# Optimization experiments

Hardware: AMD Instinct MI355X
Metric: run time of the kernel (lower is better)

## Reference

```python
import jax, jax.numpy as jnp
import numpy as np

D = 256

def setup_inputs() -> dict:
    key = jax.random.key(0)
    ks = iter(jax.random.split(key, 40))
    def nrm(shape, s=0.05):
        return (jax.random.normal(next(ks), shape, dtype=jnp.float32) * s)
    inp = {}
    inp['prot_data'] = jax.random.normal(next(ks), (8, 1000, 768), dtype=jnp.float32)
    inp['drug_data_ver'] = jax.random.normal(next(ks), (8, 56, 43), dtype=jnp.float32)
    inp['drug_data_adj'] = jax.random.uniform(next(ks), (8, 56, 56), dtype=jnp.float32)
    inp['prot_contacts'] = jax.random.uniform(next(ks), (8, 1000, 1000), dtype=jnp.float32)
    inp['prot_inter'] = jax.random.uniform(next(ks), (8, 1000, 56), dtype=jnp.float32)
    inp['prot_inter_exist'] = jax.random.uniform(next(ks), (8,), dtype=jnp.float32)
    inp['label'] = jax.random.normal(next(ks), (8, 1), dtype=jnp.float32)
    inp['fused_matrix'] = jax.random.normal(next(ks), (999, 1000), dtype=jnp.float32)
    # params
    inp['W_prot'] = nrm((768, D)); inp['b_prot'] = jnp.zeros((D,), jnp.float32)
    inp['gcn_W0'] = nrm((43, D));  inp['gcn_b0'] = jnp.zeros((D,), jnp.float32)
    inp['gcn_W1'] = nrm((D, D));   inp['gcn_b1'] = jnp.zeros((D,), jnp.float32)
    inp['gcn_W2'] = nrm((D, D));   inp['gcn_b2'] = jnp.zeros((D,), jnp.float32)
    inp['gcn_Wf'] = nrm((D, D));   inp['gcn_bf'] = jnp.zeros((D,), jnp.float32)
    inp['Wjp'] = nrm((D, D)); inp['bjp'] = jnp.zeros((D,), jnp.float32)
    inp['Wjc'] = nrm((D, D)); inp['bjc'] = jnp.zeros((D,), jnp.float32)
    inp['conv_w'] = nrm((64, 1, 4)); inp['conv_b'] = jnp.zeros((64,), jnp.float32)
    inp['W_r1'] = nrm((64 * 32, 600)); inp['b_r1'] = jnp.zeros((600,), jnp.float32)
    inp['W_r2'] = nrm((600, 300));     inp['b_r2'] = jnp.zeros((300,), jnp.float32)
    inp['W_r3'] = nrm((300, 1));       inp['b_r3'] = jnp.zeros((1,), jnp.float32)
    return inp

LAM_L1 = 1.0; LAM_FUSED = 1.0; LAM_GROUP = 1.0; LAM_BIND = 1.0

def reference(prot_data, drug_data_ver, drug_data_adj, prot_contacts, prot_inter,
              prot_inter_exist, label, fused_matrix,
              W_prot, b_prot, gcn_W0, gcn_b0, gcn_W1, gcn_b1, gcn_W2, gcn_b2,
              gcn_Wf, gcn_bf, Wjp, bjp, Wjc, bjc, conv_w, conv_b,
              W_r1, b_r1, W_r2, b_r2, W_r3, b_r3):
    # protein embedding (active path: single linear)
    prot = prot_data @ W_prot + b_prot                      # (b, 1000, 256)
    # compound GCN
    x = drug_data_ver
    for W, b in ((gcn_W0, gcn_b0), (gcn_W1, gcn_b1), (gcn_W2, gcn_b2)):
        x = jax.nn.relu(jnp.einsum('bij,bjd->bid', drug_data_adj, x @ W + b))
    comp = x @ gcn_Wf + gcn_bf                              # (b, 56, 256)
    # joint attention over prot x comp
    qp = jax.nn.relu(prot) @ Wjp + bjp
    qc = jax.nn.relu(comp) @ Wjc + bjc
    inter = jax.nn.sigmoid(jnp.einsum('bid,bkd->bik', qp, qc))  # (b, 1000, 56)
    inter = inter / jnp.sum(inter, axis=(1, 2), keepdims=True)
    # outer-product bilinear attention + weighted reduction (the 4D intermediate)
    cp4 = jnp.tanh(prot[:, :, None, :] * comp[:, None, :, :])   # (b, 1000, 56, 256)
    cp = jnp.einsum('bikd,bik->bd', cp4, inter)                 # (b, 256)
    h = cp[:, None, :]                                          # (b, 1, 256) NCH
    h = jax.lax.conv_general_dilated(h, conv_w, (2,), [(1, 1)],
                                     dimension_numbers=('NCH', 'OIH', 'NCH'))
    h = h + conv_b[None, :, None]                               # (b, 64, 128)
    h = jax.nn.leaky_relu(h, 0.1)
    h = jax.lax.reduce_window(h, -jnp.inf, jax.lax.max,
                              (1, 1, 4), (1, 1, 4), 'VALID')    # (b, 64, 32)
    h = h.reshape(h.shape[0], 64 * 32)
    h = jax.nn.leaky_relu(h @ W_r1 + b_r1, 0.1)
    h = jax.nn.leaky_relu(h @ W_r2 + b_r2, 0.1)
    affn = h @ W_r3 + b_r3                                      # (b, 1)
    # losses
    reg_l1 = jnp.mean(jnp.sum(jnp.abs(inter), axis=(1, 2)))
    reg_fused = jnp.mean(jnp.sum(jnp.abs(jnp.einsum('bij,ti->bjt', inter, fused_matrix)), axis=(1, 2)))
    group = jnp.sum(jnp.einsum('bij,bki->bjk', inter ** 2, prot_contacts), axis=1)  # (b, 1000)
    group = jnp.where(group == 0, group + 1e10, group)
    reg_group = jnp.mean(jnp.sum(jnp.sqrt(group) * jnp.sqrt(jnp.sum(prot_contacts, axis=2)), axis=1))
    loss0 = LAM_L1 * reg_l1 + LAM_FUSED * reg_fused + LAM_GROUP * reg_group
    lab_inter = prot_inter_exist[:, None, None] * prot_inter
    loss1 = jnp.mean(jnp.sqrt(jnp.sum((inter - lab_inter) ** 2, axis=(1, 2)))) * LAM_BIND
    loss2 = jnp.mean((affn - label) ** 2)
    return loss0 + loss1 + loss2
```

## Files before the change

### kernel.cpp

```cpp
#include <hip/hip_runtime.h>
#include <hip/hip_bf16.h>
#include <math.h>

#define B 8
#define NP 1000
#define NK 56
#define DP 768
#define DV 43
#define DD 256
#define NT 999

typedef __attribute__((ext_vector_type(8))) short bf16x8;
typedef __attribute__((ext_vector_type(4))) float f32x4;

__device__ inline short f2bf(float x) {
    __hip_bfloat16 h = __float2bfloat16(x);
    return __builtin_bit_cast(short, h);
}


template<bool RELU_IN>
__device__ __forceinline__ void gemm_body(
    const float* __restrict__ A, const short* __restrict__ Wb,
    const float* __restrict__ bias, float* __restrict__ C,
    int N, int K, int bm, int bn, int tid) {
    int lane = tid & 63, w = tid >> 6;
    int m0 = bm * 32 + (w >> 1) * 16;
    int n0 = bn * 128 + (w & 1) * 64;
    int lrow = lane & 15, lk = lane >> 4;
    f32x4 acc[4] = {{0.f,0.f,0.f,0.f},{0.f,0.f,0.f,0.f},
                    {0.f,0.f,0.f,0.f},{0.f,0.f,0.f,0.f}};
    const float* arow = A + (size_t)(m0 + lrow) * K + lk * 8;
    for (int k0 = 0; k0 < K; k0 += 32) {
        f32x4 a0 = *reinterpret_cast<const f32x4*>(arow + k0);
        f32x4 a1 = *reinterpret_cast<const f32x4*>(arow + k0 + 4);
        bf16x8 af;
        #pragma unroll
        for (int e = 0; e < 4; ++e) {
            float v0 = a0[e], v1 = a1[e];
            if (RELU_IN) { v0 = fmaxf(v0, 0.f); v1 = fmaxf(v1, 0.f); }
            af[e] = f2bf(v0); af[4 + e] = f2bf(v1);
        }
        const short* bbase = Wb + ((size_t)((k0 >> 3) + lk) * N + n0 + lrow) * 8;
        #pragma unroll
        for (int nt = 0; nt < 4; ++nt) {
            bf16x8 bf = *reinterpret_cast<const bf16x8*>(bbase + nt * 128);
            acc[nt] = __builtin_amdgcn_mfma_f32_16x16x32_bf16(af, bf, acc[nt], 0, 0, 0);
        }
    }
    #pragma unroll
    for (int nt = 0; nt < 4; ++nt) {
        int col = n0 + nt * 16 + lrow;
        float bv = bias[col];
        #pragma unroll
        for (int r = 0; r < 4; ++r) {
            int row = m0 + lk * 4 + r;
            C[(size_t)row * N + col] = acc[nt][r] + bv;
        }
    }
}

__device__ __forceinline__ void gcn_layer_body(
    const float* __restrict__ x, const float* __restrict__ adj,
    const float* __restrict__ W, const float* __restrict__ bias,
    float* __restrict__ y, int KIN, int bi, int tid,
    float* arow, float* u) {
    int b = bi / NK, i = bi % NK;
    if (tid < NK) arow[tid] = adj[((size_t)b * NK + i) * NK + tid];
    __syncthreads();
    if (tid < KIN) {
        float a0 = 0.f, a1 = 0.f;
        for (int j = 0; j < NK; j += 2) {
            a0 = fmaf(arow[j],     x[((size_t)b * NK + j)     * KIN + tid], a0);
            a1 = fmaf(arow[j + 1], x[((size_t)b * NK + j + 1) * KIN + tid], a1);
        }
        u[tid] = a0 + a1;
    }
    float rs = 0.f;
    for (int j = 0; j < NK; ++j) rs += arow[j];
    __syncthreads();
    float a0 = 0.f, a1 = 0.f, a2 = 0.f, a3 = 0.f;
    int kk = 0;
    for (; kk + 4 <= KIN; kk += 4) {
        a0 = fmaf(u[kk],     W[(size_t)kk * DD + tid],       a0);
        a1 = fmaf(u[kk + 1], W[(size_t)(kk + 1) * DD + tid], a1);
        a2 = fmaf(u[kk + 2], W[(size_t)(kk + 2) * DD + tid], a2);
        a3 = fmaf(u[kk + 3], W[(size_t)(kk + 3) * DD + tid], a3);
    }
    for (; kk < KIN; ++kk) a0 = fmaf(u[kk], W[(size_t)kk * DD + tid], a0);
    float v = a0 + a1 + a2 + a3 + rs * bias[tid];
    y[((size_t)b * NK + i) * DD + tid] = fmaxf(v, 0.f);
}

__device__ __forceinline__ void gcn_tail_body(
    const float* __restrict__ y1, const float* __restrict__ adj,
    const float* __restrict__ W2, const float* __restrict__ b2,
    const float* __restrict__ Wf, const float* __restrict__ bf,
    const float* __restrict__ Wjc, const float* __restrict__ bjc,
    float* __restrict__ comp, float* __restrict__ qcout,
    int bi, int tid, float* arow, float* u) {
    int b = bi / NK, i = bi % NK;
    if (tid < NK) arow[tid] = adj[((size_t)b * NK + i) * NK + tid];
    __syncthreads();
    {
        float a0 = 0.f, a1 = 0.f;
        for (int j = 0; j < NK; j += 2) {
            a0 = fmaf(arow[j],     y1[((size_t)b * NK + j)     * DD + tid], a0);
            a1 = fmaf(arow[j + 1], y1[((size_t)b * NK + j + 1) * DD + tid], a1);
        }
        u[tid] = a0 + a1;
    }
    float rs = 0.f;
    for (int j = 0; j < NK; ++j) rs += arow[j];
    __syncthreads();
    float a0 = 0.f, a1 = 0.f, a2 = 0.f, a3 = 0.f;
    #pragma unroll 4
    for (int kk = 0; kk < DD; kk += 4) {
        a0 = fmaf(u[kk],     W2[(size_t)kk * DD + tid],       a0);
        a1 = fmaf(u[kk + 1], W2[(size_t)(kk + 1) * DD + tid], a1);
        a2 = fmaf(u[kk + 2], W2[(size_t)(kk + 2) * DD + tid], a2);
        a3 = fmaf(u[kk + 3], W2[(size_t)(kk + 3) * DD + tid], a3);
    }
    float y2 = fmaxf(a0 + a1 + a2 + a3 + rs * b2[tid], 0.f);
    __syncthreads();
    u[tid] = y2;
    __syncthreads();
    a0 = a1 = a2 = a3 = 0.f;
    #pragma unroll 4
    for (int kk = 0; kk < DD; kk += 4) {
        a0 = fmaf(u[kk],     Wf[(size_t)kk * DD + tid],       a0);
        a1 = fmaf(u[kk + 1], Wf[(size_t)(kk + 1) * DD + tid], a1);
        a2 = fmaf(u[kk + 2], Wf[(size_t)(kk + 2) * DD + tid], a2);
        a3 = fmaf(u[kk + 3], Wf[(size_t)(kk + 3) * DD + tid], a3);
    }
    float cv = a0 + a1 + a2 + a3 + bf[tid];
    comp[((size_t)b * NK + i) * DD + tid] = cv;
    __syncthreads();
    u[tid] = fmaxf(cv, 0.f);
    __syncthreads();
    a0 = a1 = a2 = a3 = 0.f;
    #pragma unroll 4
    for (int kk = 0; kk < DD; kk += 4) {
        a0 = fmaf(u[kk],     Wjc[(size_t)kk * DD + tid],       a0);
        a1 = fmaf(u[kk + 1], Wjc[(size_t)(kk + 1) * DD + tid], a1);
        a2 = fmaf(u[kk + 2], Wjc[(size_t)(kk + 2) * DD + tid], a2);
        a3 = fmaf(u[kk + 3], Wjc[(size_t)(kk + 3) * DD + tid], a3);
    }
    qcout[((size_t)b * NK + i) * DD + tid] = a0 + a1 + a2 + a3 + bjc[tid];
}

__global__ __launch_bounds__(256) void k1_kernel(
    const float* __restrict__ W_prot, short* __restrict__ Wb1,
    const float* __restrict__ Wjp, short* __restrict__ Wb2,
    const float* __restrict__ fusedM, short* __restrict__ fMb,
    float* __restrict__ zero_region,
    const float* __restrict__ drug_ver, const float* __restrict__ adj,
    const float* __restrict__ W0, const float* __restrict__ b0,
    float* __restrict__ y0) {
    __shared__ float smem[2112];
    int blk = blockIdx.x, tid = threadIdx.x;
    if (blk < 96) {
        int idx = blk * 256 + tid;
        int koct = idx / DD, n = idx % DD;
        bf16x8 v;
        #pragma unroll
        for (int e = 0; e < 8; ++e)
            v[e] = f2bf(W_prot[(size_t)(koct * 8 + e) * DD + n]);
        *reinterpret_cast<bf16x8*>(Wb1 + (size_t)idx * 8) = v;
    } else if (blk < 128) {
        int idx = (blk - 96) * 256 + tid;
        int koct = idx / DD, n = idx % DD;
        bf16x8 v;
        #pragma unroll
        for (int e = 0; e < 8; ++e)
            v[e] = f2bf(Wjp[(size_t)(koct * 8 + e) * DD + n]);
        *reinterpret_cast<bf16x8*>(Wb2 + (size_t)idx * 8) = v;
    } else if (blk < 640) {
        int blk2 = blk - 128;
        int t0 = (blk2 >> 3) * 16;
        int i0 = (blk2 & 7) * 128;
        for (int l = tid; l < 16 * 128; l += 256) {
            int tt = l >> 7, ii = l & 127;
            int t = t0 + tt, i = i0 + ii;
            smem[tt * 132 + ii] = (t < NT && i < NP) ? fusedM[(size_t)t * NP + i] : 0.f;
        }
        __syncthreads();
        int octl = tid >> 4, tl = tid & 15;
        bf16x8 v;
        #pragma unroll
        for (int e = 0; e < 8; ++e)
            v[e] = f2bf(smem[tl * 132 + octl * 8 + e]);
        size_t oct = i0 / 8 + octl;
        *reinterpret_cast<bf16x8*>(fMb + (oct * 1024 + t0 + tl) * 8) = v;
    } else if (blk < 677) {
        int idx = (blk - 640) * 256 + tid;
        if (idx < 48 + B * 600 + B * 300 + B * DD) zero_region[idx] = 0.f;
    } else {
        gcn_layer_body(drug_ver, adj, W0, b0, y0, DV, blk - 677, tid,
                       smem, smem + 64);
    }
}

__global__ __launch_bounds__(256) void k2_kernel(
    const float* __restrict__ prot_data, const short* __restrict__ Wb1,
    const float* __restrict__ b_prot, float* __restrict__ prot,
    const float* __restrict__ y0, const float* __restrict__ adj,
    const float* __restrict__ W1, const float* __restrict__ b1,
    float* __restrict__ y1) {
    __shared__ float smem[320];
    int blk = blockIdx.x, tid = threadIdx.x;
    if (blk < 500)
        gemm_body<false>(prot_data, Wb1, b_prot, prot, DD, DP, blk >> 1, blk & 1, tid);
    else
        gcn_layer_body(y0, adj, W1, b1, y1, DD, blk - 500, tid, smem, smem + 64);
}

__global__ __launch_bounds__(256) void k3_kernel(
    const float* __restrict__ prot, const short* __restrict__ Wb2,
    const float* __restrict__ bjp, float* __restrict__ qp,
    const float* __restrict__ y1, const float* __restrict__ adj,
    const float* __restrict__ W2, const float* __restrict__ b2,
    const float* __restrict__ Wf, const float* __restrict__ bf,
    const float* __restrict__ Wjc, const float* __restrict__ bjc,
    float* __restrict__ comp, float* __restrict__ qc) {
    __shared__ float smem[320];
    int blk = blockIdx.x, tid = threadIdx.x;
    if (blk < 500)
        gemm_body<true>(prot, Wb2, bjp, qp, DD, DD, blk >> 1, blk & 1, tid);
    else
        gcn_tail_body(y1, adj, W2, b2, Wf, bf, Wjc, bjc, comp, qc,
                      blk - 500, tid, smem, smem + 64);
}

__global__ __launch_bounds__(256) void inter_all_kernel(
    const float* __restrict__ qp, const float* __restrict__ qc,
    const float* __restrict__ prot_inter, const float* __restrict__ exist,
    float* __restrict__ inter, float* __restrict__ s_bi,
    short* __restrict__ iTb, float* __restrict__ accums) {
    int b = blockIdx.x / 125, chunk = blockIdx.x % 125;
    __shared__ float qcT[DD * 57];
    __shared__ float qpS[8][DD];
    __shared__ float vS[8][57];
    __shared__ float wred[4][4];
    int tid = threadIdx.x;
    for (int l = tid; l < NK * DD; l += 256) {
        int k = l / DD, d = l % DD;
        qcT[d * 57 + k] = qc[((size_t)b * NK + k) * DD + d];
    }
    for (int l = tid; l < 8 * DD; l += 256) {
        int r = l >> 8, d = l & 255;
        qpS[r][d] = qp[((size_t)b * NP + chunk * 8 + r) * DD + d];
    }
    __syncthreads();
    int w = tid >> 6, lane = tid & 63;
    float ex = exist[b];
    int r0 = w * 2, r1 = w * 2 + 1;
    float acc0 = 0.f, acc1 = 0.f;
    if (lane < NK) {
        #pragma unroll 8
        for (int d = 0; d < DD; ++d) {
            float c = qcT[d * 57 + lane];
            acc0 = fmaf(qpS[r0][d], c, acc0);
            acc1 = fmaf(qpS[r1][d], c, acc1);
        }
    }
    float aV = 0.f, aA = 0.f, aC = 0.f, aD = 0.f;
    #pragma unroll
    for (int ii = 0; ii < 2; ++ii) {
        int i = chunk * 8 + w * 2 + ii;
        float v = 0.f, lab = 0.f;
        if (lane < NK) {
            float acc = (ii == 0) ? acc0 : acc1;
            v = 1.f / (1.f + __expf(-acc));
            lab = ex * prot_inter[((size_t)b * NP + i) * NK + lane];
            inter[((size_t)b * NP + i) * NK + lane] = v;
            vS[w * 2 + ii][lane] = v;
        }
        float v2 = v * v;
        float r = v2;
        #pragma unroll
        for (int off = 32; off; off >>= 1) r += __shfl_down(r, off);
        if (lane == 0) s_bi[(size_t)b * NP + i] = r;
        aV += v; aA += v2; aC += v * lab; aD += lab * lab;
    }
    #pragma unroll
    for (int off = 32; off; off >>= 1) {
        aV += __shfl_down(aV, off);
        aA += __shfl_down(aA, off);
        aC += __shfl_down(aC, off);
        aD += __shfl_down(aD, off);
    }
    if (lane == 0) {
        wred[w][0] = aV; wred[w][1] = aA; wred[w][2] = aC; wred[w][3] = aD;
    }
    __syncthreads();
    if (tid < 4) {
        float s = wred[0][tid] + wred[1][tid] + wred[2][tid] + wred[3][tid];
        atomicAdd(&accums[tid * 8 + b], s);
    }
    if (tid < NK) {
        bf16x8 pk;
        #pragma unroll
        for (int e = 0; e < 8; ++e) pk[e] = f2bf(vS[e][tid]);
        *reinterpret_cast<bf16x8*>(iTb + ((size_t)chunk * 448 + b * NK + tid) * 8) = pk;
        if (chunk == 124) {
            bf16x8 z = {0,0,0,0,0,0,0,0};
            #pragma unroll
            for (int oct = 125; oct < 128; ++oct)
                *reinterpret_cast<bf16x8*>(iTb + ((size_t)oct * 448 + b * NK + tid) * 8) = z;
        }
    }
}

__global__ __launch_bounds__(256) void k5_kernel(
    const float* __restrict__ prot, const float* __restrict__ comp,
    const float* __restrict__ inter, float* __restrict__ cp,
    const short* __restrict__ iTb, const short* __restrict__ fMb,
    float* __restrict__ fusedAbs,
    const float* __restrict__ contacts, const float* __restrict__ s_bi,
    const float* __restrict__ accums, float* __restrict__ groupv) {
    __shared__ float irow[8][NK];
    __shared__ float sb[8];
    int blk = blockIdx.x, tid = threadIdx.x;
    if (blk < 1000) {
        int b = blk / 125, chunk = blk % 125;
        int d = tid;
        float creg[NK];
        #pragma unroll
        for (int k = 0; k < NK; ++k)
            creg[k] = comp[((size_t)b * NK + k) * DD + d];
        for (int l = tid; l < 8 * NK; l += 256) {
            int ii = l / NK, k = l % NK;
            irow[ii][k] = inter[((size_t)b * NP + chunk * 8 + ii) * NK + k];
        }
        const float C2LOG2E = 2.8853900817779268f;
        float p2l[8];
        #pragma unroll
        for (int ii = 0; ii < 8; ++ii)
            p2l[ii] = C2LOG2E * prot[((size_t)b * NP + chunk * 8 + ii) * DD + d];
        __syncthreads();
        float acc0 = 0.f, acc1 = 0.f;
        #pragma unroll 1
        for (int ii = 0; ii < 8; ++ii) {
            float p = p2l[ii];
            #pragma unroll
            for (int k = 0; k < NK; k += 2) {
                float e0 = __builtin_amdgcn_exp2f(p * creg[k]);
                float e1 = __builtin_amdgcn_exp2f(p * creg[k + 1]);
                float r0 = __builtin_amdgcn_rcpf(e0 + 1.f);
                float r1 = __builtin_amdgcn_rcpf(e1 + 1.f);
                acc0 = fmaf(fmaf(-2.f, r0, 1.f), irow[ii][k],     acc0);
                acc1 = fmaf(fmaf(-2.f, r1, 1.f), irow[ii][k + 1], acc1);
            }
        }
        atomicAdd(&cp[(size_t)b * DD + d], acc0 + acc1);
    } else if (blk < 1112) {
        int fblk = blk - 1000;
        int mb = fblk % 14, nb = fblk / 14;
        int lane = tid & 63, w = tid >> 6;
        if (tid < 8) sb[tid] = 0.f;
        __syncthreads();
        int m0 = mb * 32 + (w >> 1) * 16;
        int n0 = nb * 128 + (w & 1) * 64;
        int lrow = lane & 15, lk = lane >> 4;
        f32x4 acc[4] = {{0.f,0.f,0.f,0.f},{0.f,0.f,0.f,0.f},
                        {0.f,0.f,0.f,0.f},{0.f,0.f,0.f,0.f}};
        for (int koct0 = 0; koct0 < 128; koct0 += 4) {
            int koct = koct0 + lk;
            bf16x8 af = *reinterpret_cast<const bf16x8*>(
                iTb + ((size_t)koct * 448 + m0 + lrow) * 8);
            const short* bb = fMb + ((size_t)koct * 1024 + n0 + lrow) * 8;
            #pragma unroll
            for (int nt = 0; nt < 4; ++nt) {
                bf16x8 bf = *reinterpret_cast<const bf16x8*>(bb + nt * 128);
                acc[nt] = __builtin_amdgcn_mfma_f32_16x16x32_bf16(af, bf, acc[nt], 0, 0, 0);
            }
        }
        #pragma unroll
        for (int r = 0; r < 4; ++r) {
            float part = fabsf(acc[0][r]) + fabsf(acc[1][r]) +
                         fabsf(acc[2][r]) + fabsf(acc[3][r]);
            #pragma unroll
            for (int off = 1; off < 16; off <<= 1)
                part += __shfl_xor(part, off);
            if (lrow == 0) {
                int row = m0 + lk * 4 + r;
                atomicAdd(&sb[row / NK], part);
            }
        }
        __syncthreads();
        if (tid < 8 && sb[tid] != 0.f) atomicAdd(&fusedAbs[tid], sb[tid]);
    } else {
        int w = tid >> 6, lane = tid & 63;
        int gk = (blk - 1112) * 4 + w;
        int b = gk / NP;
        const f32x4* row4 = reinterpret_cast<const f32x4*>(
            contacts + (size_t)gk * NP);
        const f32x4* sv4 = reinterpret_cast<const f32x4*>(s_bi + (size_t)b * NP);
        f32x4 z = {0.f, 0.f, 0.f, 0.f};
        f32x4 c0 = row4[lane];
        f32x4 c1 = row4[lane + 64];
        f32x4 c2 = row4[lane + 128];
        f32x4 c3 = z, s3 = z;
        f32x4 s0 = sv4[lane];
        f32x4 s1 = sv4[lane + 64];
        f32x4 s2 = sv4[lane + 128];
        if (lane + 192 < 250) { c3 = row4[lane + 192]; s3 = sv4[lane + 192]; }
        float g0 = 0.f, g1 = 0.f, g2 = 0.f, g3 = 0.f;
        #pragma unroll
        for (int e = 0; e < 4; ++e) {
            g0 = fmaf(c0[e], s0[e], g0);
            g1 = fmaf(c1[e], s1[e], g1);
            g2 = fmaf(c2[e], s2[e], g2);
            g3 = fmaf(c3[e], s3[e], g3);
        }
        float r0 = (c0[0] + c0[1]) + (c0[2] + c0[3]);
        float r1 = (c1[0] + c1[1]) + (c1[2] + c1[3]);
        float r2 = (c2[0] + c2[1]) + (c2[2] + c2[3]);
        float r3 = (c3[0] + c3[1]) + (c3[2] + c3[3]);
        float g = (g0 + g1) + (g2 + g3);
        float rs = (r0 + r1) + (r2 + r3);
        #pragma unroll
        for (int off = 32; off; off >>= 1) {
            g += __shfl_down(g, off);
            rs += __shfl_down(rs, off);
        }
        if (lane == 0) {
            float val;
            if (g == 0.f) val = sqrtf(1e10f) * sqrtf(rs);
            else          val = sqrtf(g) / accums[b] * sqrtf(rs);
            groupv[gk] = val;
        }
    }
}

__global__ __launch_bounds__(256) void convpool_kernel(
    const float* __restrict__ cp, const float* __restrict__ accums,
    const float* __restrict__ conv_w, const float* __restrict__ conv_b,
    float* __restrict__ pooled) {
    int b = blockIdx.x, t = threadIdx.x;
    __shared__ float xS[258];
    __shared__ float convo[8192];
    float invS = 1.f / accums[b];
    xS[t + 1] = cp[(size_t)b * DD + t] * invS;
    if (t == 0) { xS[0] = 0.f; xS[257] = 0.f; }
    __syncthreads();
    for (int l = t; l < 8192; l += 256) {
        int o = l >> 7, pos = l & 127;
        float acc = conv_b[o];
        int base = pos * 2;
        #pragma unroll
        for (int h = 0; h < 4; ++h)
            acc = fmaf(xS[base + h], conv_w[o * 4 + h], acc);
        convo[l] = (acc > 0.f) ? acc : 0.1f * acc;
    }
    __syncthreads();
    for (int l = t; l < 2048; l += 256) {
        int o = l >> 5, p = l & 31;
        float m = convo[o * 128 + p * 4];
        m = fmaxf(m, convo[o * 128 + p * 4 + 1]);
        m = fmaxf(m, convo[o * 128 + p * 4 + 2]);
        m = fmaxf(m, convo[o * 128 + p * 4 + 3]);
        pooled[b * 2048 + l] = m;
    }
}

template<bool FIN>
__global__ __launch_bounds__(256) void fc_partial_kernel(
    const float* __restrict__ in, const float* __restrict__ bias_in,
    const float* __restrict__ W, float* __restrict__ raw,
    int K, int N, int kchunk) {
    int t = threadIdx.x;
    int ol = t & 63;
    int o = blockIdx.x * 64 + ol;
    int w = t >> 6;
    int kbeg = blockIdx.y * kchunk;
    int kend = kbeg + kchunk; if (kend > K) kend = K;
    int len = kend - kbeg;
    __shared__ float sin_[B][128];
    for (int l = t; l < B * len; l += 256) {
        int b = l / len, k = l % len;
        float v = in[(size_t)b * K + kbeg + k];
        if (FIN) {
            v += bias_in[kbeg + k];
            v = (v > 0.f) ? v : 0.1f * v;
        }
        sin_[b][k] = v;
    }
    __syncthreads();
    float acc[B];
    #pragma unroll
    for (int b = 0; b < B; ++b) acc[b] = 0.f;
    if (o < N) {
        for (int k = kbeg + w; k < kend; k += 4) {
            float wv = W[(size_t)k * N + o];
            int kl = k - kbeg;
            #pragma unroll
            for (int b = 0; b < B; ++b)
                acc[b] = fmaf(sin_[b][kl], wv, acc[b]);
        }
    }
    __shared__ float red[4][64][B];
    #pragma unroll
    for (int b = 0; b < B; ++b) red[w][ol][b] = acc[b];
    __syncthreads();
    for (int p = t; p < 64 * B; p += 256) {
        int oo = p / B, b = p % B;
        int o2 = blockIdx.x * 64 + oo;
        if (o2 < N) {
            float s = red[0][oo][b] + red[1][oo][b] + red[2][oo][b] + red[3][oo][b];
            atomicAdd(&raw[(size_t)b * N + o2], s);
        }
    }
}

__global__ __launch_bounds__(256) void final_kernel(
    const float* __restrict__ accums, const float* __restrict__ groupv,
    const float* __restrict__ raw2, const float* __restrict__ b_r2,
    const float* __restrict__ W3, const float* __restrict__ b3,
    const float* __restrict__ label, float* __restrict__ out) {
    int tid = threadIdx.x;
    __shared__ float affnS[8];
    {
        int b = tid >> 5, k0 = tid & 31;
        float acc = 0.f;
        for (int k = k0; k < 300; k += 32) {
            float v = raw2[(size_t)b * 300 + k] + b_r2[k];
            v = (v > 0.f) ? v : 0.1f * v;
            acc = fmaf(v, W3[k], acc);
        }
        #pragma unroll
        for (int off = 16; off; off >>= 1) acc += __shfl_down(acc, off);
        if (k0 == 0) affnS[b] = acc + b3[0];
    }
    float s = 0.f;
    for (int l = tid; l < B * NP; l += 256) s += groupv[l];
    __shared__ float r[256];
    r[tid] = s;
    __syncthreads();
    for (int st = 128; st; st >>= 1) {
        if (tid < st) r[tid] += r[tid + st];
        __syncthreads();
    }
    if (tid == 0) {
        float gtot = r[0];
        float l0 = 0.f, l1 = 0.f, l2 = 0.f;
        for (int b = 0; b < B; ++b) {
            float S = accums[b];
            float A = accums[8 + b], C = accums[16 + b], D = accums[24 + b];
            float fA = accums[32 + b];
            l0 += 1.f + fA / S;
            float bind = A / (S * S) - 2.f * C / S + D;
            l1 += sqrtf(fmaxf(bind, 0.f));
            float dd = affnS[b] - label[b];
            l2 += dd * dd;
        }
        out[0] = (l0 + gtot + l1 + l2) * 0.125f;
    }
}

extern "C" void kernel_launch(void* const* d_in, const int* in_sizes, int n_in,
                              void* d_out, int out_size, void* d_ws, size_t ws_size,
                              hipStream_t stream) {
    const float* prot_data   = (const float*)d_in[0];
    const float* drug_ver    = (const float*)d_in[1];
    const float* drug_adj    = (const float*)d_in[2];
    const float* contacts    = (const float*)d_in[3];
    const float* prot_inter  = (const float*)d_in[4];
    const float* exist       = (const float*)d_in[5];
    const float* label       = (const float*)d_in[6];
    const float* fused       = (const float*)d_in[7];
    const float* W_prot      = (const float*)d_in[8];
    const float* b_prot      = (const float*)d_in[9];
    const float* gcn_W0      = (const float*)d_in[10];
    const float* gcn_b0      = (const float*)d_in[11];
    const float* gcn_W1      = (const float*)d_in[12];
    const float* gcn_b1      = (const float*)d_in[13];
    const float* gcn_W2      = (const float*)d_in[14];
    const float* gcn_b2      = (const float*)d_in[15];
    const float* gcn_Wf      = (const float*)d_in[16];
    const float* gcn_bf      = (const float*)d_in[17];
    const float* Wjp         = (const float*)d_in[18];
    const float* bjp         = (const float*)d_in[19];
    const float* Wjc         = (const float*)d_in[20];
    const float* bjc         = (const float*)d_in[21];
    const float* conv_w      = (const float*)d_in[22];
    const float* conv_b      = (const float*)d_in[23];
    const float* W_r1        = (const float*)d_in[24];
    const float* b_r1        = (const float*)d_in[25];
    const float* W_r2        = (const float*)d_in[26];
    const float* b_r2        = (const float*)d_in[27];
    const float* W_r3        = (const float*)d_in[28];
    const float* b_r3        = (const float*)d_in[29];

    float* ws = (float*)d_ws;
    size_t off = 0;
    auto alloc = [&](size_t n) { float* p = ws + off; off += n; return p; };
    float* prot     = alloc((size_t)B * NP * DD);
    float* qp       = alloc((size_t)B * NP * DD);
    float* tbuf     = alloc((size_t)B * NK * DD);
    float* ybuf     = alloc((size_t)B * NK * DD);
    float* comp     = alloc((size_t)B * NK * DD);
    float* qc       = alloc((size_t)B * NK * DD);
    float* inter    = alloc((size_t)B * NP * NK);
    float* s_bi     = alloc((size_t)B * NP);
    float* pooled   = alloc((size_t)B * 2048);
    float* groupv   = alloc((size_t)B * NP);
    short* Wb1      = (short*)alloc((DP / 8) * DD * 8 / 2);
    short* Wb2      = (short*)alloc((DD / 8) * DD * 8 / 2);
    short* fMb      = (short*)alloc((size_t)128 * 1024 * 8 / 2);
    float* accums   = alloc(48);
    float* raw1     = alloc((size_t)B * 600);
    float* raw2     = alloc((size_t)B * 300);
    float* cp       = alloc((size_t)B * DD);

    short* iTb = (short*)tbuf;
    (void)ybuf;

    k1_kernel<<<1125, 256, 0, stream>>>(W_prot, Wb1, Wjp, Wb2, fused, fMb,
                                        accums, drug_ver, drug_adj,
                                        gcn_W0, gcn_b0, tbuf);

    k2_kernel<<<948, 256, 0, stream>>>(prot_data, Wb1, b_prot, prot,
                                       tbuf, drug_adj, gcn_W1, gcn_b1, ybuf);

    k3_kernel<<<948, 256, 0, stream>>>(prot, Wb2, bjp, qp,
                                       ybuf, drug_adj, gcn_W2, gcn_b2,
                                       gcn_Wf, gcn_bf, Wjc, bjc, comp, qc);

    inter_all_kernel<<<B * 125, 256, 0, stream>>>(
        qp, qc, prot_inter, exist, inter, s_bi, iTb, accums);

    k5_kernel<<<3112, 256, 0, stream>>>(prot, comp, inter, cp,
                                        iTb, fMb, accums + 32,
                                        contacts, s_bi, accums, groupv);

    convpool_kernel<<<B, 256, 0, stream>>>(cp, accums, conv_w, conv_b, pooled);

    fc_partial_kernel<false><<<dim3(10, 16), 256, 0, stream>>>(
        pooled, nullptr, W_r1, raw1, 2048, 600, 128);
    fc_partial_kernel<true><<<dim3(5, 8), 256, 0, stream>>>(
        raw1, b_r1, W_r2, raw2, 600, 300, 75);

    final_kernel<<<1, 256, 0, stream>>>(accums, groupv, raw2, b_r2,
                                        W_r3, b_r3, label, (float*)d_out);
}
```

Before: 162.9 us.

## Fuse conv+pool into FC1 kernel, specialize FC kernels, prefetch GEMM A loads

Removes the separate conv/pool kernel. Each FC1 block now recomputes the conv, leaky-relu and max-pool values it needs straight from cp into shared memory, which drops one launch and the pooled buffer round trip. The FC kernels get compile-time constant sizes, and the GEMM body software-prefetches the next A tile into registers. In exchange the conv work is recomputed redundantly across the 10 column blocks, and the prefetch raises register use.

```diff
diff --git a/kernel.cpp b/kernel.cpp
--- a/kernel.cpp
+++ b/kernel.cpp
@@ -31,13 +31,18 @@
     f32x4 acc[4] = {{0.f,0.f,0.f,0.f},{0.f,0.f,0.f,0.f},
                     {0.f,0.f,0.f,0.f},{0.f,0.f,0.f,0.f}};
     const float* arow = A + (size_t)(m0 + lrow) * K + lk * 8;
+    f32x4 a0 = *reinterpret_cast<const f32x4*>(arow);
+    f32x4 a1 = *reinterpret_cast<const f32x4*>(arow + 4);
     for (int k0 = 0; k0 < K; k0 += 32) {
-        f32x4 a0 = *reinterpret_cast<const f32x4*>(arow + k0);
-        f32x4 a1 = *reinterpret_cast<const f32x4*>(arow + k0 + 4);
+        f32x4 c0 = a0, c1 = a1;
+        if (k0 + 32 < K) {
+            a0 = *reinterpret_cast<const f32x4*>(arow + k0 + 32);
+            a1 = *reinterpret_cast<const f32x4*>(arow + k0 + 36);
+        }
         bf16x8 af;
         #pragma unroll
         for (int e = 0; e < 4; ++e) {
-            float v0 = a0[e], v1 = a1[e];
+            float v0 = c0[e], v1 = c1[e];
             if (RELU_IN) { v0 = fmaxf(v0, 0.f); v1 = fmaxf(v1, 0.f); }
             af[e] = f2bf(v0); af[4 + e] = f2bf(v1);
         }
@@ -434,57 +439,82 @@
     }
 }
 
-__global__ __launch_bounds__(256) void convpool_kernel(
+__global__ __launch_bounds__(256) void fc1_conv_kernel(
     const float* __restrict__ cp, const float* __restrict__ accums,
     const float* __restrict__ conv_w, const float* __restrict__ conv_b,
-    float* __restrict__ pooled) {
-    int b = blockIdx.x, t = threadIdx.x;
-    __shared__ float xS[258];
-    __shared__ float convo[8192];
-    float invS = 1.f / accums[b];
-    xS[t + 1] = cp[(size_t)b * DD + t] * invS;
-    if (t == 0) { xS[0] = 0.f; xS[257] = 0.f; }
-    __syncthreads();
-    for (int l = t; l < 8192; l += 256) {
-        int o = l >> 7, pos = l & 127;
-        float acc = conv_b[o];
-        int base = pos * 2;
-        #pragma unroll
-        for (int h = 0; h < 4; ++h)
-            acc = fmaf(xS[base + h], conv_w[o * 4 + h], acc);
-        convo[l] = (acc > 0.f) ? acc : 0.1f * acc;
-    }
-    __syncthreads();
-    for (int l = t; l < 2048; l += 256) {
-        int o = l >> 5, p = l & 31;
-        float m = convo[o * 128 + p * 4];
-        m = fmaxf(m, convo[o * 128 + p * 4 + 1]);
-        m = fmaxf(m, convo[o * 128 + p * 4 + 2]);
-        m = fmaxf(m, convo[o * 128 + p * 4 + 3]);
-        pooled[b * 2048 + l] = m;
-    }
-}
-
-template<bool FIN>
-__global__ __launch_bounds__(256) void fc_partial_kernel(
-    const float* __restrict__ in, const float* __restrict__ bias_in,
-    const float* __restrict__ W, float* __restrict__ raw,
-    int K, int N, int kchunk) {
+    const float* __restrict__ W, float* __restrict__ raw) {
+    const int K = 2048, N = 600, kchunk = 128;
     int t = threadIdx.x;
     int ol = t & 63;
     int o = blockIdx.x * 64 + ol;
     int w = t >> 6;
     int kbeg = blockIdx.y * kchunk;
-    int kend = kbeg + kchunk; if (kend > K) kend = K;
-    int len = kend - kbeg;
+    __shared__ float xS[B][258];
     __shared__ float sin_[B][128];
-    for (int l = t; l < B * len; l += 256) {
-        int b = l / len, k = l % len;
-        float v = in[(size_t)b * K + kbeg + k];
-        if (FIN) {
-            v += bias_in[kbeg + k];
-            v = (v > 0.f) ? v : 0.1f * v;
-        }
+    for (int l = t; l < B * DD; l += 256) {
+        int b = l >> 8, d = l & 255;
+        xS[b][d + 1] = cp[(size_t)b * DD + d] / accums[b];
+    }
+    if (t < B) { xS[t][0] = 0.f; xS[t][257] = 0.f; }
+    __syncthreads();
+    for (int l = t; l < B * kchunk; l += 256) {
+        int b = l >> 7, kl = l & 127;
+        int kg = kbeg + kl;
+        int oo = kg >> 5, p = kg & 31;
+        float w0 = conv_w[oo * 4 + 0], w1 = conv_w[oo * 4 + 1];
+        float w2 = conv_w[oo * 4 + 2], w3 = conv_w[oo * 4 + 3];
+        float cb = conv_b[oo];
+        float m = -INFINITY;
+        #pragma unroll
+        for (int q = 0; q < 4; ++q) {
+            int base = (p * 4 + q) * 2;
+            float acc = cb;
+            acc = fmaf(xS[b][base + 0], w0, acc);
+            acc = fmaf(xS[b][base + 1], w1, acc);
+            acc = fmaf(xS[b][base + 2], w2, acc);
+            acc = fmaf(xS[b][base + 3], w3, acc);
+            acc = (acc > 0.f) ? acc : 0.1f * acc;
+            m = fmaxf(m, acc);
+        }
+        sin_[b][kl] = m;
+    }
+    __syncthreads();
+    float acc[B];
+    #pragma unroll
+    for (int b = 0; b < B; ++b) acc[b] = 0.f;
+    for (int k = kbeg + w; k < kbeg + kchunk; k += 4) {
+        float wv = W[(size_t)k * N + o];
+        int kl = k - kbeg;
+        #pragma unroll
+        for (int b = 0; b < B; ++b)
+            acc[b] = fmaf(sin_[b][kl], wv, acc[b]);
+    }
+    __shared__ float red[4][64][B];
+    #pragma unroll
+    for (int b = 0; b < B; ++b) red[w][ol][b] = acc[b];
+    __syncthreads();
+    for (int p = t; p < 64 * B; p += 256) {
+        int oo = p / B, b = p % B;
+        int o2 = blockIdx.x * 64 + oo;
+        float s = red[0][oo][b] + red[1][oo][b] + red[2][oo][b] + red[3][oo][b];
+        atomicAdd(&raw[(size_t)b * N + o2], s);
+    }
+}
+
+__global__ __launch_bounds__(256) void fc2_kernel(
+    const float* __restrict__ raw1, const float* __restrict__ b_r1,
+    const float* __restrict__ W, float* __restrict__ raw2) {
+    const int K = 600, N = 300, kchunk = 75;
+    int t = threadIdx.x;
+    int ol = t & 63;
+    int o = blockIdx.x * 64 + ol;
+    int w = t >> 6;
+    int kbeg = blockIdx.y * kchunk;
+    __shared__ float sin_[B][128];
+    for (int l = t; l < B * kchunk; l += 256) {
+        int b = l / kchunk, k = l % kchunk;
+        float v = raw1[(size_t)b * K + kbeg + k] + b_r1[kbeg + k];
+        v = (v > 0.f) ? v : 0.1f * v;
         sin_[b][k] = v;
     }
     __syncthreads();
@@ -492,7 +522,7 @@
     #pragma unroll
     for (int b = 0; b < B; ++b) acc[b] = 0.f;
     if (o < N) {
-        for (int k = kbeg + w; k < kend; k += 4) {
+        for (int k = kbeg + w; k < kbeg + kchunk; k += 4) {
             float wv = W[(size_t)k * N + o];
             int kl = k - kbeg;
             #pragma unroll
@@ -509,7 +539,7 @@
         int o2 = blockIdx.x * 64 + oo;
         if (o2 < N) {
             float s = red[0][oo][b] + red[1][oo][b] + red[2][oo][b] + red[3][oo][b];
-            atomicAdd(&raw[(size_t)b * N + o2], s);
+            atomicAdd(&raw2[(size_t)b * N + o2], s);
         }
     }
 }
@@ -604,7 +634,6 @@
     float* qc       = alloc((size_t)B * NK * DD);
     float* inter    = alloc((size_t)B * NP * NK);
     float* s_bi     = alloc((size_t)B * NP);
-    float* pooled   = alloc((size_t)B * 2048);
     float* groupv   = alloc((size_t)B * NP);
     short* Wb1      = (short*)alloc((DP / 8) * DD * 8 / 2);
     short* Wb2      = (short*)alloc((DD / 8) * DD * 8 / 2);
@@ -635,12 +664,10 @@
                                         iTb, fMb, accums + 32,
                                         contacts, s_bi, accums, groupv);
 
-    convpool_kernel<<<B, 256, 0, stream>>>(cp, accums, conv_w, conv_b, pooled);
-
-    fc_partial_kernel<false><<<dim3(10, 16), 256, 0, stream>>>(
-        pooled, nullptr, W_r1, raw1, 2048, 600, 128);
-    fc_partial_kernel<true><<<dim3(5, 8), 256, 0, stream>>>(
-        raw1, b_r1, W_r2, raw2, 600, 300, 75);
+    fc1_conv_kernel<<<dim3(10, 16), 256, 0, stream>>>(
+        cp, accums, conv_w, conv_b, W_r1, raw1);
+
+    fc2_kernel<<<dim3(5, 8), 256, 0, stream>>>(raw1, b_r1, W_r2, raw2);
 
     final_kernel<<<1, 256, 0, stream>>>(accums, groupv, raw2, b_r2,
                                         W_r3, b_r3, label, (float*)d_out);
```

Measured after the change: 160.7 us. About the same (-1.4%).
